# Optimization experiments

Measured on AMD Instinct MI355X. Metric: run time of the kernel, lower is better.

Reference implementation:

```python
import jax, jax.numpy as jnp
import numpy as np

WIN = 9
PAD = WIN // 2    # floor(9/2) = 4
WIN_SIZE = WIN * WIN
EPS = 1e-05


def _box_sum(x):
    # 9x9 ones-kernel conv, stride 1, pad 4 (SAME size), NCHW with C=1
    filt = jnp.ones((1, 1, WIN, WIN), dtype=x.dtype)
    return jax.lax.conv_general_dilated(
        x, filt, window_strides=(1, 1),
        padding=[(PAD, PAD), (PAD, PAD)],
        dimension_numbers=('NCHW', 'OIHW', 'NCHW'))


def setup_inputs() -> dict:
    key = jax.random.key(0)
    k1, k2 = jax.random.split(key)
    I = jax.random.normal(k1, (8, 1, 1024, 1024), dtype=jnp.float32)
    J = jax.random.normal(k2, (8, 1, 1024, 1024), dtype=jnp.float32)
    return {"I": I, "J": J}


def reference(I, J):
    I_sum = _box_sum(I)
    J_sum = _box_sum(J)
    I2_sum = _box_sum(I * I)
    J2_sum = _box_sum(J * J)
    IJ_sum = _box_sum(I * J)

    u_I = I_sum / WIN_SIZE
    u_J = J_sum / WIN_SIZE

    cross = IJ_sum - u_J * I_sum - u_I * J_sum + u_I * u_J * WIN_SIZE
    I_var = I2_sum - 2 * u_I * I_sum + u_I * u_I * WIN_SIZE
    J_var = J2_sum - 2 * u_J * J_sum + u_J * u_J * WIN_SIZE

    cc = cross * cross / (I_var * J_var + EPS)
    return jnp.mean(cc)
```

## Files before the change

kernel.cpp:

```cpp
#include <hip/hip_runtime.h>

#define H 1024
#define W 1024
#define NIMG 8
#define CPT 4
#define TH 16
#define NBX 4
#define WPB 4
#define NBY (H / (TH * WPB))
#define NWAVES (NBX * NBY * NIMG * WPB)
#define EPS 1e-5f

struct RS { float I[CPT], J[CPT], II[CPT], JJ[CPT], IJ[CPT]; };

__device__ __forceinline__ void row_rs(const float* __restrict__ Irow,
                                       const float* __restrict__ Jrow,
                                       int X, bool okL, bool okR, RS& o) {
  float a[12], b[12];
  { float4 q = *reinterpret_cast<const float4*>(Irow + X);
    a[4]=q.x; a[5]=q.y; a[6]=q.z; a[7]=q.w;
    float4 p = *reinterpret_cast<const float4*>(Jrow + X);
    b[4]=p.x; b[5]=p.y; b[6]=p.z; b[7]=p.w; }
  if (okL) {
    float4 q = *reinterpret_cast<const float4*>(Irow + X - 4);
    a[0]=q.x; a[1]=q.y; a[2]=q.z; a[3]=q.w;
    float4 p = *reinterpret_cast<const float4*>(Jrow + X - 4);
    b[0]=p.x; b[1]=p.y; b[2]=p.z; b[3]=p.w;
  } else { a[0]=a[1]=a[2]=a[3]=0.f; b[0]=b[1]=b[2]=b[3]=0.f; }
  if (okR) {
    float4 q = *reinterpret_cast<const float4*>(Irow + X + 4);
    a[8]=q.x; a[9]=q.y; a[10]=q.z; a[11]=q.w;
    float4 p = *reinterpret_cast<const float4*>(Jrow + X + 4);
    b[8]=p.x; b[9]=p.y; b[10]=p.z; b[11]=p.w;
  } else { a[8]=a[9]=a[10]=a[11]=0.f; b[8]=b[9]=b[10]=b[11]=0.f; }

  float sI=0.f, sJ=0.f, sII=0.f, sJJ=0.f, sIJ=0.f;
  #pragma unroll
  for (int k = 0; k < 9; ++k) {
    sI += a[k]; sJ += b[k];
    sII = fmaf(a[k], a[k], sII);
    sJJ = fmaf(b[k], b[k], sJJ);
    sIJ = fmaf(a[k], b[k], sIJ);
  }
  o.I[0]=sI; o.J[0]=sJ; o.II[0]=sII; o.JJ[0]=sJJ; o.IJ[0]=sIJ;
  #pragma unroll
  for (int i = 1; i < CPT; ++i) {
    float an=a[i+8], al=a[i-1], bn=b[i+8], bl=b[i-1];
    sI += an - al;  sJ += bn - bl;
    sII = fmaf(-al, al, fmaf(an, an, sII));
    sJJ = fmaf(-bl, bl, fmaf(bn, bn, sJJ));
    sIJ = fmaf(-al, bl, fmaf(an, bn, sIJ));
    o.I[i]=sI; o.J[i]=sJ; o.II[i]=sII; o.JJ[i]=sJJ; o.IJ[i]=sIJ;
  }
}

__global__ __launch_bounds__(256, 2)
void ncc_main(const float* __restrict__ I, const float* __restrict__ J,
              float* __restrict__ partial) {
  const int tid  = threadIdx.x;
  const int lane = tid & 63, wv = tid >> 6;
  const int X  = blockIdx.x * 256 + lane * CPT;
  const int y0 = (blockIdx.y * WPB + wv) * TH;
  const bool okL = (X >= 4);
  const bool okR = (X + 8 <= W);
  const size_t img_off = (size_t)blockIdx.z * H * W;
  const float* Ip = I + img_off;
  const float* Jp = J + img_off;

  float wI[CPT], wJ[CPT], wII[CPT], wJJ[CPT], wIJ[CPT];
  #pragma unroll
  for (int i = 0; i < CPT; ++i) { wI[i]=wJ[i]=wII[i]=wJJ[i]=wIJ[i]=0.f; }
  float acc = 0.f;
  const float inv81 = 1.0f / 81.0f;

  auto apply = [&](int r, float sgn) {
    if ((unsigned)r < (unsigned)H) {
      RS o;
      row_rs(Ip + (size_t)r * W, Jp + (size_t)r * W, X, okL, okR, o);
      #pragma unroll
      for (int i = 0; i < CPT; ++i) {
        wI[i]  = fmaf(sgn, o.I[i],  wI[i]);
        wJ[i]  = fmaf(sgn, o.J[i],  wJ[i]);
        wII[i] = fmaf(sgn, o.II[i], wII[i]);
        wJJ[i] = fmaf(sgn, o.JJ[i], wJJ[i]);
        wIJ[i] = fmaf(sgn, o.IJ[i], wIJ[i]);
      }
    }
  };
  auto emit = [&]() {
    #pragma unroll
    for (int i = 0; i < CPT; ++i) {
      float cross = fmaf(-(wI[i] * wJ[i]), inv81, wIJ[i]);
      float Iv    = fmaf(-(wI[i] * wI[i]), inv81, wII[i]);
      float Jv    = fmaf(-(wJ[i] * wJ[i]), inv81, wJJ[i]);
      acc = fmaf(cross * cross,
                 __builtin_amdgcn_rcpf(fmaf(Iv, Jv, EPS)), acc);
    }
  };

  for (int k = 0; k < 8; ++k) apply(y0 - 4 + k, 1.0f);
  apply(y0 + 4, 1.0f);
  emit();
  for (int k = 0; k < TH - 1; ++k) {
    apply(y0 + 5 + k, 1.0f);
    apply(y0 - 4 + k, -1.0f);
    emit();
  }

  #pragma unroll
  for (int off = 32; off > 0; off >>= 1)
    acc += __shfl_down(acc, off, 64);
  if (lane == 0) {
    const int wid = (((int)blockIdx.z * NBY + (int)blockIdx.y) * NBX
                     + (int)blockIdx.x) * WPB + wv;
    partial[wid] = acc;
  }
}

__global__ __launch_bounds__(256)
void ncc_reduce(const float* __restrict__ partial, float* __restrict__ out) {
  __shared__ float red[4];
  const int tid = threadIdx.x;
  const float4* p4 = reinterpret_cast<const float4*>(partial);
  float s = 0.f;
  #pragma unroll
  for (int i = tid; i < NWAVES / 4; i += 256) {
    float4 v = p4[i];
    s += (v.x + v.y) + (v.z + v.w);
  }
  #pragma unroll
  for (int off = 32; off > 0; off >>= 1)
    s += __shfl_down(s, off, 64);
  if ((tid & 63) == 0) red[tid >> 6] = s;
  __syncthreads();
  if (tid == 0)
    out[0] = (red[0] + red[1] + red[2] + red[3]) *
             (1.0f / (float)((size_t)NIMG * H * W));
}

extern "C" void kernel_launch(void* const* d_in, const int* in_sizes, int n_in,
                              void* d_out, int out_size, void* d_ws, size_t ws_size,
                              hipStream_t stream) {
  const float* I = (const float*)d_in[0];
  const float* J = (const float*)d_in[1];
  float* out     = (float*)d_out;
  float* partial = (float*)d_ws;

  dim3 grid(NBX, NBY, NIMG);
  hipLaunchKernelGGL(ncc_main, grid, dim3(256), 0, stream, I, J, partial);
  hipLaunchKernelGGL(ncc_reduce, dim3(1), dim3(256), 0, stream, partial, out);
}
```

Measured before the change: 111.0 us.

## Switch to vertical-first column sums with 8 columns per thread

Reorders the separable box sum so each thread keeps vertical running sums for 16 columns (5 moments) and derives the horizontal 9-wide sums per output row from those registers, instead of recomputing horizontal row sums for every added and removed row. Each thread now covers 8 output columns, and blocks shrink to a single 64-lane wave, giving a grid of 2x64x8 = 1024 waves. Row loads are issued in pairs ahead of the accumulation to overlap memory latency. The larger register footprint and smaller total wave count risk lower occupancy and weaker latency hiding.

```diff
diff --git a/kernel.cpp b/kernel.cpp
--- a/kernel.cpp
+++ b/kernel.cpp
@@ -3,116 +3,122 @@
 #define H 1024
 #define W 1024
 #define NIMG 8
-#define CPT 4
+#define CPT 8
+#define VC 16
 #define TH 16
-#define NBX 4
-#define WPB 4
-#define NBY (H / (TH * WPB))
-#define NWAVES (NBX * NBY * NIMG * WPB)
+#define NBANDS (H / TH)
+#define NWAVES (2 * NBANDS * NIMG)
 #define EPS 1e-5f
 
-struct RS { float I[CPT], J[CPT], II[CPT], JJ[CPT], IJ[CPT]; };
-
-__device__ __forceinline__ void row_rs(const float* __restrict__ Irow,
-                                       const float* __restrict__ Jrow,
-                                       int X, bool okL, bool okR, RS& o) {
-  float a[12], b[12];
-  { float4 q = *reinterpret_cast<const float4*>(Irow + X);
-    a[4]=q.x; a[5]=q.y; a[6]=q.z; a[7]=q.w;
-    float4 p = *reinterpret_cast<const float4*>(Jrow + X);
-    b[4]=p.x; b[5]=p.y; b[6]=p.z; b[7]=p.w; }
-  if (okL) {
-    float4 q = *reinterpret_cast<const float4*>(Irow + X - 4);
-    a[0]=q.x; a[1]=q.y; a[2]=q.z; a[3]=q.w;
-    float4 p = *reinterpret_cast<const float4*>(Jrow + X - 4);
-    b[0]=p.x; b[1]=p.y; b[2]=p.z; b[3]=p.w;
-  } else { a[0]=a[1]=a[2]=a[3]=0.f; b[0]=b[1]=b[2]=b[3]=0.f; }
-  if (okR) {
-    float4 q = *reinterpret_cast<const float4*>(Irow + X + 4);
-    a[8]=q.x; a[9]=q.y; a[10]=q.z; a[11]=q.w;
-    float4 p = *reinterpret_cast<const float4*>(Jrow + X + 4);
-    b[8]=p.x; b[9]=p.y; b[10]=p.z; b[11]=p.w;
-  } else { a[8]=a[9]=a[10]=a[11]=0.f; b[8]=b[9]=b[10]=b[11]=0.f; }
-
-  float sI=0.f, sJ=0.f, sII=0.f, sJJ=0.f, sIJ=0.f;
-  #pragma unroll
-  for (int k = 0; k < 9; ++k) {
-    sI += a[k]; sJ += b[k];
-    sII = fmaf(a[k], a[k], sII);
-    sJJ = fmaf(b[k], b[k], sJJ);
-    sIJ = fmaf(a[k], b[k], sIJ);
-  }
-  o.I[0]=sI; o.J[0]=sJ; o.II[0]=sII; o.JJ[0]=sJJ; o.IJ[0]=sIJ;
-  #pragma unroll
-  for (int i = 1; i < CPT; ++i) {
-    float an=a[i+8], al=a[i-1], bn=b[i+8], bl=b[i-1];
-    sI += an - al;  sJ += bn - bl;
-    sII = fmaf(-al, al, fmaf(an, an, sII));
-    sJJ = fmaf(-bl, bl, fmaf(bn, bn, sJJ));
-    sIJ = fmaf(-al, bl, fmaf(an, bn, sIJ));
-    o.I[i]=sI; o.J[i]=sJ; o.II[i]=sII; o.JJ[i]=sJJ; o.IJ[i]=sIJ;
-  }
+__device__ __forceinline__ float4 ld4(const float* p) {
+  return *reinterpret_cast<const float4*>(p);
 }
 
-__global__ __launch_bounds__(256, 2)
+struct Row { float4 i0,i1,i2,i3, j0,j1,j2,j3; };
+
+__device__ __forceinline__ void load_row(const float* __restrict__ Ir,
+                                         const float* __restrict__ Jr,
+                                         int xl, int X, int xr, Row& o) {
+  o.i0 = ld4(Ir + xl); o.i1 = ld4(Ir + X); o.i2 = ld4(Ir + X + 4); o.i3 = ld4(Ir + xr);
+  o.j0 = ld4(Jr + xl); o.j1 = ld4(Jr + X); o.j2 = ld4(Jr + X + 4); o.j3 = ld4(Jr + xr);
+}
+
+__global__ __launch_bounds__(64, 1)
 void ncc_main(const float* __restrict__ I, const float* __restrict__ J,
               float* __restrict__ partial) {
-  const int tid  = threadIdx.x;
-  const int lane = tid & 63, wv = tid >> 6;
-  const int X  = blockIdx.x * 256 + lane * CPT;
-  const int y0 = (blockIdx.y * WPB + wv) * TH;
+  const int lane = threadIdx.x;
+  const int xh   = blockIdx.x;
+  const int band = blockIdx.y;
+  const int n    = blockIdx.z;
+  const int X  = xh * 512 + lane * CPT;
+  const int y0 = band * TH;
   const bool okL = (X >= 4);
-  const bool okR = (X + 8 <= W);
-  const size_t img_off = (size_t)blockIdx.z * H * W;
-  const float* Ip = I + img_off;
-  const float* Jp = J + img_off;
+  const bool okR = (X + 12 <= W);
+  const int xl = okL ? X - 4 : X;
+  const int xr = okR ? X + 8 : X + 4;
+  const float* Ip = I + (size_t)n * H * W;
+  const float* Jp = J + (size_t)n * H * W;
 
-  float wI[CPT], wJ[CPT], wII[CPT], wJJ[CPT], wIJ[CPT];
+  float vI[VC], vJ[VC], vII[VC], vJJ[VC], vIJ[VC];
   #pragma unroll
-  for (int i = 0; i < CPT; ++i) { wI[i]=wJ[i]=wII[i]=wJJ[i]=wIJ[i]=0.f; }
+  for (int c = 0; c < VC; ++c) { vI[c]=vJ[c]=vII[c]=vJJ[c]=vIJ[c]=0.f; }
   float acc = 0.f;
   const float inv81 = 1.0f / 81.0f;
 
-  auto apply = [&](int r, float sgn) {
-    if ((unsigned)r < (unsigned)H) {
-      RS o;
-      row_rs(Ip + (size_t)r * W, Jp + (size_t)r * W, X, okL, okR, o);
-      #pragma unroll
-      for (int i = 0; i < CPT; ++i) {
-        wI[i]  = fmaf(sgn, o.I[i],  wI[i]);
-        wJ[i]  = fmaf(sgn, o.J[i],  wJ[i]);
-        wII[i] = fmaf(sgn, o.II[i], wII[i]);
-        wJJ[i] = fmaf(sgn, o.JJ[i], wJJ[i]);
-        wIJ[i] = fmaf(sgn, o.IJ[i], wIJ[i]);
+  auto accum = [&](const Row& r, float sgn) {
+    float a[VC], b[VC];
+    a[0]=okL?r.i0.x:0.f; a[1]=okL?r.i0.y:0.f; a[2]=okL?r.i0.z:0.f; a[3]=okL?r.i0.w:0.f;
+    b[0]=okL?r.j0.x:0.f; b[1]=okL?r.j0.y:0.f; b[2]=okL?r.j0.z:0.f; b[3]=okL?r.j0.w:0.f;
+    a[4]=r.i1.x; a[5]=r.i1.y; a[6]=r.i1.z; a[7]=r.i1.w;
+    b[4]=r.j1.x; b[5]=r.j1.y; b[6]=r.j1.z; b[7]=r.j1.w;
+    a[8]=r.i2.x; a[9]=r.i2.y; a[10]=r.i2.z; a[11]=r.i2.w;
+    b[8]=r.j2.x; b[9]=r.j2.y; b[10]=r.j2.z; b[11]=r.j2.w;
+    a[12]=okR?r.i3.x:0.f; a[13]=okR?r.i3.y:0.f; a[14]=okR?r.i3.z:0.f; a[15]=okR?r.i3.w:0.f;
+    b[12]=okR?r.j3.x:0.f; b[13]=okR?r.j3.y:0.f; b[14]=okR?r.j3.z:0.f; b[15]=okR?r.j3.w:0.f;
+    #pragma unroll
+    for (int c = 0; c < VC; ++c) {
+      float sa = sgn * a[c];
+      vI[c]  += sa;
+      vJ[c]  = fmaf(sgn, b[c], vJ[c]);
+      vII[c] = fmaf(sa, a[c], vII[c]);
+      vJJ[c] = fmaf(sgn * b[c], b[c], vJJ[c]);
+      vIJ[c] = fmaf(sa, b[c], vIJ[c]);
+    }
+  };
+
+  auto emitrow = [&]() {
+    float hI=0.f, hJ=0.f, hII=0.f, hJJ=0.f, hIJ=0.f;
+    #pragma unroll
+    for (int k = 0; k < 9; ++k) {
+      hI += vI[k]; hJ += vJ[k]; hII += vII[k]; hJJ += vJJ[k]; hIJ += vIJ[k];
+    }
+    #pragma unroll
+    for (int c = 0; c < CPT; ++c) {
+      float cross = fmaf(-(hI * hJ), inv81, hIJ);
+      float Iv    = fmaf(-(hI * hI), inv81, hII);
+      float Jv    = fmaf(-(hJ * hJ), inv81, hJJ);
+      acc = fmaf(cross * cross,
+                 __builtin_amdgcn_rcpf(fmaf(Iv, Jv, EPS)), acc);
+      if (c < CPT - 1) {
+        hI  += vI[c+9]  - vI[c];   hJ  += vJ[c+9]  - vJ[c];
+        hII += vII[c+9] - vII[c];  hJJ += vJJ[c+9] - vJJ[c];
+        hIJ += vIJ[c+9] - vIJ[c];
       }
     }
   };
-  auto emit = [&]() {
-    #pragma unroll
-    for (int i = 0; i < CPT; ++i) {
-      float cross = fmaf(-(wI[i] * wJ[i]), inv81, wIJ[i]);
-      float Iv    = fmaf(-(wI[i] * wI[i]), inv81, wII[i]);
-      float Jv    = fmaf(-(wJ[i] * wJ[i]), inv81, wJJ[i]);
-      acc = fmaf(cross * cross,
-                 __builtin_amdgcn_rcpf(fmaf(Iv, Jv, EPS)), acc);
-    }
-  };
 
-  for (int k = 0; k < 8; ++k) apply(y0 - 4 + k, 1.0f);
-  apply(y0 + 4, 1.0f);
-  emit();
-  for (int k = 0; k < TH - 1; ++k) {
-    apply(y0 + 5 + k, 1.0f);
-    apply(y0 - 4 + k, -1.0f);
-    emit();
+  #pragma unroll 1
+  for (int k = 0; k < 9; k += 2) {
+    const int r1 = y0 - 4 + k, r2 = r1 + 1;
+    const bool v1 = (unsigned)r1 < (unsigned)H;
+    const bool v2 = (k + 1 < 9) && ((unsigned)r2 < (unsigned)H);
+    Row A, B;
+    if (v1) load_row(Ip + (size_t)r1 * W, Jp + (size_t)r1 * W, xl, X, xr, A);
+    if (v2) load_row(Ip + (size_t)r2 * W, Jp + (size_t)r2 * W, xl, X, xr, B);
+    if (v1) accum(A, 1.0f);
+    if (v2) accum(B, 1.0f);
   }
+
+  #pragma unroll 1
+  for (int y = y0; y < y0 + TH - 1; ++y) {
+    const int re = y + 5;
+    const int rl = y - 4;
+    const bool ev = re < H;
+    const bool lv = rl >= 0;
+    Row E, L;
+    if (ev) load_row(Ip + (size_t)re * W, Jp + (size_t)re * W, xl, X, xr, E);
+    if (lv) load_row(Ip + (size_t)rl * W, Jp + (size_t)rl * W, xl, X, xr, L);
+    emitrow();
+    if (ev) accum(E,  1.0f);
+    if (lv) accum(L, -1.0f);
+  }
+  emitrow();
 
   #pragma unroll
   for (int off = 32; off > 0; off >>= 1)
     acc += __shfl_down(acc, off, 64);
   if (lane == 0) {
-    const int wid = (((int)blockIdx.z * NBY + (int)blockIdx.y) * NBX
-                     + (int)blockIdx.x) * WPB + wv;
+    const int wid = ((int)n * NBANDS + band) * 2 + xh;
     partial[wid] = acc;
   }
 }
@@ -146,7 +152,7 @@
   float* out     = (float*)d_out;
   float* partial = (float*)d_ws;
 
-  dim3 grid(NBX, NBY, NIMG);
-  hipLaunchKernelGGL(ncc_main, grid, dim3(256), 0, stream, I, J, partial);
+  dim3 grid(2, NBANDS, NIMG);
+  hipLaunchKernelGGL(ncc_main, grid, dim3(64), 0, stream, I, J, partial);
   hipLaunchKernelGGL(ncc_reduce, dim3(1), dim3(256), 0, stream, partial, out);
 }
```

Result: slower. 121.9 us (+9.8%).
